# Performance work log

Hardware: AMD Instinct MI355X
Metric: run time of the kernel (lower is better)

## Reference

```python
import jax, jax.numpy as jnp
import numpy as np

EPS = 1e-4            # EDM2 normalize() epsilon
NUM_HEADS = 12
ATTN_BALANCE = 0.3
ROPE_BASE = 10000.0
NEG_INF = -1e9


def mp_weight(w):
    """EDM2 MPConv weight: per-output-channel normalize + magnitude-preserving scale.
    w: [out, in] (1x1 conv kernel squeezed)."""
    fan_in = w.shape[1]
    norm = jnp.linalg.norm(w, axis=1, keepdims=True)
    w = w / (EPS + norm * np.float32(np.sqrt(1.0 / fan_in)))  # normalize()
    return w * np.float32(1.0 / np.sqrt(fan_in))              # gain/sqrt(fan_in), gain=1


def apply_rope(q, k):
    """Rotary embedding over the frame index t. q,k: [b, m, t, hw, d]."""
    d = q.shape[-1]
    t = q.shape[2]
    inv_freq = 1.0 / (ROPE_BASE ** (jnp.arange(0, d, 2, dtype=jnp.float32) / d))
    ang = jnp.arange(t, dtype=jnp.float32)[:, None] * inv_freq[None, :]   # [t, d/2]
    cos = jnp.cos(ang)[None, None, :, None, :].astype(q.dtype)
    sin = jnp.sin(ang)[None, None, :, None, :].astype(q.dtype)

    def rot(x):
        x1, x2 = jnp.split(x, 2, axis=-1)
        return jnp.concatenate([x1 * cos - x2 * sin, x1 * sin + x2 * cos], axis=-1)

    return rot(q), rot(k)


def video_attention(x, w_qkv, w_proj, batch_size):
    bt, C, h, w_ = x.shape
    b = batch_size
    t = bt // b
    m = NUM_HEADS
    c = C // m
    hw = h * w_
    S = t * hw

    # MPConv QKV (1x1 conv == channel matmul)
    y = jnp.einsum('oi,bihw->bohw', mp_weight(w_qkv), x)   # [(b t), 3C, h, w]
    # '(b t) (s m c) h w -> s b m t (h w) c'
    y = y.reshape(b, t, 3, m, c, h, w_).transpose(2, 0, 3, 1, 5, 6, 4).reshape(3, b, m, t, hw, c)
    q, k, v = y[0], y[1], y[2]

    q, k = apply_rope(q, k)
    q = q.reshape(b, m, S, c)
    k = k.reshape(b, m, S, c)
    v = v.reshape(b, m, S, c)

    # block-causal video mask: token in frame i attends to all tokens of frames <= i
    frame = jnp.arange(S) // hw
    mask = frame[:, None] >= frame[None, :]                 # [S, S]

    scores = jnp.einsum('bmqc,bmkc->bmqk', q, k) * np.float32(1.0 / np.sqrt(c))
    scores = jnp.where(mask, scores, NEG_INF)
    attn = jax.nn.softmax(scores, axis=-1)
    yo = jnp.einsum('bmqk,bmkc->bmqc', attn, v)             # [b, m, S, c]

    # 'b m (t h w) c -> (b t) (c m) h w'
    yo = yo.reshape(b, m, t, h, w_, c).transpose(0, 2, 5, 1, 3, 4).reshape(bt, C, h, w_)
    yo = jnp.einsum('oi,bihw->bohw', mp_weight(w_proj), yo)

    # mp_sum(x, y, t=attn_balance)
    tb = ATTN_BALANCE
    scale = np.float32(1.0 / np.sqrt((1.0 - tb) ** 2 + tb ** 2))
    return (x * np.float32(1.0 - tb) + yo * np.float32(tb)) * scale


def setup_inputs() -> dict:
    key = jax.random.key(0)
    k1, k2, k3 = jax.random.split(key, 3)
    batch_size = 2
    n_frames = 8
    C, h, w = 768, 16, 16
    x = jax.random.normal(k1, (batch_size * n_frames, C, h, w), dtype=jnp.float32)
    w_qkv = jax.random.normal(k2, (3 * C, C), dtype=jnp.float32)
    w_proj = jax.random.normal(k3, (C, C), dtype=jnp.float32)
    return {"x": x, "w_qkv": w_qkv, "w_proj": w_proj, "batch_size": batch_size}


def reference(x, w_qkv, w_proj, batch_size):
    return video_attention(x, w_qkv, w_proj, batch_size)
```

## Files before the change

kernel.cpp:

```cpp
#include <hip/hip_runtime.h>

typedef __bf16 bf16_t;
typedef __bf16 bf16x4 __attribute__((ext_vector_type(4)));
typedef __bf16 bf16x8 __attribute__((ext_vector_type(8)));
typedef float  f32x4  __attribute__((ext_vector_type(4)));

static constexpr int NHEADS = 12, HC = 64, HW = 256, SEQ = 2048;
static constexpr size_t QKV_ONE = (size_t)2 * NHEADS * SEQ * HC;
static constexpr size_t NSTRIDE = 768 * 256;

__global__ __launch_bounds__(256) void va_prep(const float* __restrict__ wqkv,
                                               const float* __restrict__ wproj,
                                               const float* __restrict__ x,
                                               bf16_t* __restrict__ wout,
                                               bf16_t* __restrict__ xt) {
    int blk = blockIdx.x;
    if (blk < 3072) {
        int row = blk;
        bool is_proj = (row >= 2304);
        const float* wr = is_proj ? wproj + (size_t)(row - 2304) * 768
                                  : wqkv + (size_t)row * 768;
        float part = 0.f;
        for (int i = threadIdx.x; i < 768; i += 256) { float v = wr[i]; part += v * v; }
#pragma unroll
        for (int off = 32; off > 0; off >>= 1) part += __shfl_down(part, off, 64);
        __shared__ float red[4];
        if ((threadIdx.x & 63) == 0) red[threadIdx.x >> 6] = part;
        __syncthreads();
        if (threadIdx.x == 0) {
            float s = red[0] + red[1] + red[2] + red[3];
            red[0] = 1.0f / (2.7712813e-3f + sqrtf(s));
        }
        __syncthreads();
        float sc = red[0];
        for (int i = threadIdx.x; i < 768; i += 256) {
            int j = is_proj ? ((i % 12) * 64 + i / 12) : i;
            wout[(size_t)row * 768 + j] = (bf16_t)(wr[i] * sc);
        }
    } else {
        int t = blk - 3072;
        int n  = t & 15;
        int rest = t >> 4;
        int p0 = (rest & 7) * 32;
        int c0 = (rest >> 3) * 32;
        __shared__ float sm[32][33];
        int tx = threadIdx.x & 31, ty = threadIdx.x >> 5;
        const float* xp = x + (size_t)n * NSTRIDE;
#pragma unroll
        for (int i = 0; i < 4; i++)
            sm[ty + i * 8][tx] = xp[(size_t)(c0 + ty + i * 8) * 256 + p0 + tx];
        __syncthreads();
        bf16_t* xo = xt + (size_t)n * NSTRIDE;
#pragma unroll
        for (int i = 0; i < 4; i++)
            xo[(size_t)(p0 + ty + i * 8) * 768 + c0 + tx] = (bf16_t)sm[tx][ty + i * 8];
    }
}

__global__ __launch_bounds__(256, 2) void va_qkv_mfma(const bf16_t* __restrict__ Wb,
                                                      const bf16_t* __restrict__ xt,
                                                      bf16_t* __restrict__ qkvb) {
    int idx = blockIdx.x;
    int n  = (idx & 7) + 8 * ((idx >> 3) & 1);
    int rest = idx >> 4;
    int p0 = (rest & 1) * 128;
    int m0 = (rest >> 1) * 128;
    int tid = threadIdx.x;
    int lane = tid & 63, w = tid >> 6;
    int lo = lane & 15, hi = lane >> 4;
    int wm = w >> 1, wn = w & 1;
    int lx = lo & 7;

    __shared__ bf16_t Asm[128 * 64];
    __shared__ bf16_t Bsm[128 * 64];

    int srow = tid >> 3, schunk = tid & 7;
    const bf16_t* Ag = Wb + (size_t)(m0 + srow) * 768 + schunk * 8;
    const bf16_t* Bg = xt + (size_t)n * NSTRIDE + (size_t)(p0 + srow) * 768 + schunk * 8;
    int sdst = srow * 128 + ((schunk ^ (srow & 7)) << 4);

    f32x4 acc[4][4];
#pragma unroll
    for (int mt = 0; mt < 4; mt++)
#pragma unroll
        for (int nt = 0; nt < 4; nt++) acc[mt][nt] = (f32x4){0.f, 0.f, 0.f, 0.f};

    bf16x8 sa[4], sb[4];

    auto gload = [&](int k0) {
#pragma unroll
        for (int i = 0; i < 4; i++) {
            sa[i] = *(const bf16x8*)(Ag + (size_t)i * 32 * 768 + k0);
            sb[i] = *(const bf16x8*)(Bg + (size_t)i * 32 * 768 + k0);
        }
    };
    auto swrite = [&]() {
        char* Ac = (char*)Asm;
        char* Bc = (char*)Bsm;
#pragma unroll
        for (int i = 0; i < 4; i++) {
            *(bf16x8*)(Ac + sdst + i * 32 * 128) = sa[i];
            *(bf16x8*)(Bc + sdst + i * 32 * 128) = sb[i];
        }
    };

    gload(0);
    for (int s = 0; s < 12; s++) {
        __syncthreads();
        swrite();
        if (s < 11) gload((s + 1) * 64);
        __syncthreads();
#pragma unroll
        for (int kk = 0; kk < 64; kk += 32) {
            int cb = kk >> 3;
            bf16x8 af[4], bfr[4];
            const char* Ac = (const char*)Asm;
            const char* Bc = (const char*)Bsm;
#pragma unroll
            for (int mt = 0; mt < 4; mt++) {
                int row = wm * 64 + mt * 16 + lo;
                af[mt] = *(const bf16x8*)(Ac + row * 128 + (((cb + hi) ^ lx) << 4));
            }
#pragma unroll
            for (int nt = 0; nt < 4; nt++) {
                int row = wn * 64 + nt * 16 + lo;
                bfr[nt] = *(const bf16x8*)(Bc + row * 128 + (((cb + hi) ^ lx) << 4));
            }
#pragma unroll
            for (int mt = 0; mt < 4; mt++)
#pragma unroll
                for (int nt = 0; nt < 4; nt++)
                    acc[mt][nt] = __builtin_amdgcn_mfma_f32_16x16x32_bf16(af[mt], bfr[nt], acc[mt][nt], 0, 0, 0);
        }
    }

    int head_global = (m0 + wm * 64) >> 6;
    int qkv_idx = head_global / 12;
    int head    = head_global % 12;
    int b = n >> 3, tt = n & 7;
    int bm = b * 12 + head;
    if (qkv_idx < 2) {
        float qsc = (qkv_idx == 0) ? 0.18033688011f : 1.0f;
        float ttf = (float)tt;
#pragma unroll
        for (int mt = 0; mt < 2; mt++)
#pragma unroll
            for (int r = 0; r < 4; r++) {
                int j = mt * 16 + hi * 4 + r;
                float ang = ttf * __expf(-(float)j * 0.2878231366242557f);
                float cs = __cosf(ang), sn = __sinf(ang);
#pragma unroll
                for (int nt = 0; nt < 4; nt++) {
                    float x1 = acc[mt][nt][r], x2 = acc[mt + 2][nt][r];
                    acc[mt][nt][r]     = (x1 * cs - x2 * sn) * qsc;
                    acc[mt + 2][nt][r] = (x1 * sn + x2 * cs) * qsc;
                }
            }
        bf16_t* dst = qkvb + (size_t)qkv_idx * QKV_ONE + ((size_t)bm * SEQ + (size_t)tt * HW) * HC;
#pragma unroll
        for (int mt = 0; mt < 4; mt++)
#pragma unroll
            for (int nt = 0; nt < 4; nt++)
#pragma unroll
                for (int r = 0; r < 4; r++) {
                    int cc = mt * 16 + hi * 4 + r;
                    int p  = p0 + wn * 64 + nt * 16 + lo;
                    dst[(size_t)p * HC + cc] = (bf16_t)acc[mt][nt][r];
                }
    } else {
        bf16_t* dst = qkvb + 2 * QKV_ONE + (size_t)bm * HC * SEQ + (size_t)tt * HW;
#pragma unroll
        for (int mt = 0; mt < 4; mt++)
#pragma unroll
            for (int nt = 0; nt < 4; nt++)
#pragma unroll
                for (int r = 0; r < 4; r++) {
                    int cc = mt * 16 + hi * 4 + r;
                    int p  = p0 + wn * 64 + nt * 16 + lo;
                    dst[(size_t)cc * SEQ + p] = (bf16_t)acc[mt][nt][r];
                }
    }
}

__global__ __launch_bounds__(256, 2) void va_attn(const bf16_t* __restrict__ qkvb,
                                                  bf16_t* __restrict__ yob) {
    int s = blockIdx.x;
    int f = 7 - (s / 96);
    int within = s % 96;
    int bm = within % 24;
    int qs = within / 24;

    int tid = threadIdx.x;
    int w = tid >> 6, lane = tid & 63;
    int lo = lane & 15, hi = lane >> 4;
    int lx = lo & 7;

    const bf16_t* qbase = qkvb + (size_t)bm * SEQ * HC;
    const bf16_t* kbase = qkvb + QKV_ONE + (size_t)bm * SEQ * HC;
    const bf16_t* vbase = qkvb + 2 * QKV_ONE + (size_t)bm * HC * SEQ;

    __shared__ bf16_t PBF[4][64 * 64];
    __shared__ float  Lsm[4][64];
    bf16_t* PBw = PBF[w];

    const bf16_t* qrow = qbase + (size_t)(f * 256 + qs * 64 + lo) * HC;
    bf16x8 qf[4][2];
#pragma unroll
    for (int nq = 0; nq < 4; nq++) {
        qf[nq][0] = *(const bf16x8*)(qrow + (size_t)nq * 16 * HC + hi * 8);
        qf[nq][1] = *(const bf16x8*)(qrow + (size_t)nq * 16 * HC + 32 + hi * 8);
    }
    f32x4 o[4][4];
#pragma unroll
    for (int ct = 0; ct < 4; ct++)
#pragma unroll
        for (int nq = 0; nq < 4; nq++) o[ct][nq] = (f32x4){0.f, 0.f, 0.f, 0.f};
    float l4[4] = {0.f, 0.f, 0.f, 0.f};

    int kend = (f + 1) * 256;

    bf16x8 ka[8];
    {
        const bf16_t* kp = kbase + (size_t)(w * 64 + lo) * HC + hi * 8;
#pragma unroll
        for (int mt = 0; mt < 4; mt++) {
            ka[2 * mt]     = *(const bf16x8*)(kp + (size_t)mt * 16 * HC);
            ka[2 * mt + 1] = *(const bf16x8*)(kp + (size_t)mt * 16 * HC + 32);
        }
    }

    for (int kpos = w * 64; kpos < kend; kpos += 256) {
        const bf16_t* vp = vbase + (size_t)(lo) * SEQ + kpos + hi * 8;
        bf16x8 va[8];
#pragma unroll
        for (int ct = 0; ct < 4; ct++) {
            va[2 * ct]     = *(const bf16x8*)(vp + (size_t)ct * 16 * SEQ);
            va[2 * ct + 1] = *(const bf16x8*)(vp + (size_t)ct * 16 * SEQ + 32);
        }
        __builtin_amdgcn_s_setprio(1);
#pragma unroll
        for (int mt = 0; mt < 2; mt++) {
#pragma unroll
            for (int nq = 0; nq < 4; nq++) {
                f32x4 sacc = (f32x4){0.f, 0.f, 0.f, 0.f};
                sacc = __builtin_amdgcn_mfma_f32_16x16x32_bf16(ka[2 * mt], qf[nq][0], sacc, 0, 0, 0);
                sacc = __builtin_amdgcn_mfma_f32_16x16x32_bf16(ka[2 * mt + 1], qf[nq][1], sacc, 0, 0, 0);
                bf16x4 pk;
#pragma unroll
                for (int r = 0; r < 4; r++) {
                    float p;
                    asm("v_exp_f32 %0, %1" : "=v"(p) : "v"(sacc[r]));
                    l4[nq] += p;
                    pk[r] = (bf16_t)p;
                }
                *(bf16x4*)(PBw + (nq * 16 + lo) * 64 +
                           (((2 * mt + (hi >> 1)) ^ lx) * 8) + (hi & 1) * 4) = pk;
            }
        }
        __builtin_amdgcn_s_setprio(0);
        bf16x8 pb0[4], pb1[4];
#pragma unroll
        for (int nq = 0; nq < 4; nq++)
            pb0[nq] = *(const bf16x8*)(PBw + (nq * 16 + lo) * 64 + (hi ^ lx) * 8);
        __builtin_amdgcn_s_setprio(1);
#pragma unroll
        for (int mt = 2; mt < 4; mt++) {
#pragma unroll
            for (int nq = 0; nq < 4; nq++) {
                f32x4 sacc = (f32x4){0.f, 0.f, 0.f, 0.f};
                sacc = __builtin_amdgcn_mfma_f32_16x16x32_bf16(ka[2 * mt], qf[nq][0], sacc, 0, 0, 0);
                sacc = __builtin_amdgcn_mfma_f32_16x16x32_bf16(ka[2 * mt + 1], qf[nq][1], sacc, 0, 0, 0);
                bf16x4 pk;
#pragma unroll
                for (int r = 0; r < 4; r++) {
                    float p;
                    asm("v_exp_f32 %0, %1" : "=v"(p) : "v"(sacc[r]));
                    l4[nq] += p;
                    pk[r] = (bf16_t)p;
                }
                *(bf16x4*)(PBw + (nq * 16 + lo) * 64 +
                           (((2 * mt + (hi >> 1)) ^ lx) * 8) + (hi & 1) * 4) = pk;
            }
        }
        __builtin_amdgcn_s_setprio(0);
        int knext = (kpos + 256 < kend) ? kpos + 256 : kpos;
        bf16x8 kan[8];
        {
            const bf16_t* kp = kbase + (size_t)(knext + lo) * HC + hi * 8;
#pragma unroll
            for (int mt = 0; mt < 4; mt++) {
                kan[2 * mt]     = *(const bf16x8*)(kp + (size_t)mt * 16 * HC);
                kan[2 * mt + 1] = *(const bf16x8*)(kp + (size_t)mt * 16 * HC + 32);
            }
        }
#pragma unroll
        for (int nq = 0; nq < 4; nq++)
            pb1[nq] = *(const bf16x8*)(PBw + (nq * 16 + lo) * 64 + ((4 + hi) ^ lx) * 8);
        __builtin_amdgcn_s_setprio(1);
#pragma unroll
        for (int ct = 0; ct < 4; ct++)
#pragma unroll
            for (int nq = 0; nq < 4; nq++)
                o[ct][nq] = __builtin_amdgcn_mfma_f32_16x16x32_bf16(va[2 * ct], pb0[nq], o[ct][nq], 0, 0, 0);
#pragma unroll
        for (int ct = 0; ct < 4; ct++)
#pragma unroll
            for (int nq = 0; nq < 4; nq++)
                o[ct][nq] = __builtin_amdgcn_mfma_f32_16x16x32_bf16(va[2 * ct + 1], pb1[nq], o[ct][nq], 0, 0, 0);
        __builtin_amdgcn_s_setprio(0);
#pragma unroll
        for (int i = 0; i < 8; i++) ka[i] = kan[i];
    }
#pragma unroll
    for (int nq = 0; nq < 4; nq++) {
        l4[nq] += __shfl_xor(l4[nq], 16, 64);
        l4[nq] += __shfl_xor(l4[nq], 32, 64);
    }
    if (hi == 0) {
#pragma unroll
        for (int nq = 0; nq < 4; nq++) Lsm[w][nq * 16 + lo] = l4[nq];
    }
#pragma unroll
    for (int ct = 0; ct < 4; ct++)
#pragma unroll
        for (int nq = 0; nq < 4; nq++) {
            bf16x4 ov;
#pragma unroll
            for (int r = 0; r < 4; r++) ov[r] = (bf16_t)o[ct][nq][r];
            *(bf16x4*)(PBw + (nq * 16 + lo) * 64 +
                       (((2 * ct + (hi >> 1)) ^ lx) * 8) + (hi & 1) * 4) = ov;
        }
    __syncthreads();
    int head = bm % 12, b = bm / 12;
    bf16_t* yb = yob + (size_t)(b * 8 + f) * NSTRIDE + (size_t)(qs * 64) * 768 + head * 64;
#pragma unroll
    for (int i = 0; i < 2; i++) {
        int c = i * 256 + tid;
        int row = c >> 3, j = c & 7;
        int off = row * 64 + ((j ^ (row & 7)) * 8);
        float invl = 1.0f / (Lsm[0][row] + Lsm[1][row] + Lsm[2][row] + Lsm[3][row]);
        bf16x8 p0 = *(const bf16x8*)(PBF[0] + off);
        bf16x8 p1 = *(const bf16x8*)(PBF[1] + off);
        bf16x8 p2 = *(const bf16x8*)(PBF[2] + off);
        bf16x8 p3 = *(const bf16x8*)(PBF[3] + off);
        bf16x8 o8;
#pragma unroll
        for (int r = 0; r < 8; r++)
            o8[r] = (bf16_t)(((float)p0[r] + (float)p1[r] + (float)p2[r] + (float)p3[r]) * invl);
        *(bf16x8*)(yb + (size_t)row * 768 + j * 8) = o8;
    }
}

__global__ __launch_bounds__(256, 2) void va_proj_mfma(const bf16_t* __restrict__ Wb,
                                                       const bf16_t* __restrict__ yob,
                                                       const float* __restrict__ x,
                                                       float* __restrict__ out) {
    int idx = blockIdx.x;
    int n  = (idx & 7) + 8 * ((idx >> 3) & 1);
    int rest = idx >> 4;
    int p0 = (rest & 1) * 128;
    int m0 = (rest >> 1) * 64;
    int tid = threadIdx.x;
    int lane = tid & 63, w = tid >> 6;
    int lo = lane & 15, hi = lane >> 4;
    int lx = lo & 7;

    __shared__ bf16_t Asm[64 * 64];
    __shared__ bf16_t Bsm[128 * 64];

    int srow = tid >> 3, schunk = tid & 7;
    const bf16_t* Ag = Wb + (size_t)(m0 + srow) * 768 + schunk * 8;
    const bf16_t* Bg = yob + (size_t)n * NSTRIDE + (size_t)(p0 + srow) * 768 + schunk * 8;
    int sdst = srow * 128 + ((schunk ^ (srow & 7)) << 4);

    f32x4 acc[4][2];
#pragma unroll
    for (int mt = 0; mt < 4; mt++)
#pragma unroll
        for (int nt = 0; nt < 2; nt++) acc[mt][nt] = (f32x4){0.f, 0.f, 0.f, 0.f};

    bf16x8 sa[2], sb[4];
    auto gload = [&](int k0) {
#pragma unroll
        for (int i = 0; i < 2; i++)
            sa[i] = *(const bf16x8*)(Ag + (size_t)i * 32 * 768 + k0);
#pragma unroll
        for (int i = 0; i < 4; i++)
            sb[i] = *(const bf16x8*)(Bg + (size_t)i * 32 * 768 + k0);
    };
    auto swrite = [&]() {
        char* Ac = (char*)Asm;
        char* Bc = (char*)Bsm;
#pragma unroll
        for (int i = 0; i < 2; i++)
            *(bf16x8*)(Ac + sdst + i * 32 * 128) = sa[i];
#pragma unroll
        for (int i = 0; i < 4; i++)
            *(bf16x8*)(Bc + sdst + i * 32 * 128) = sb[i];
    };

    gload(0);
    for (int s = 0; s < 12; s++) {
        __syncthreads();
        swrite();
        if (s < 11) gload((s + 1) * 64);
        __syncthreads();
#pragma unroll
        for (int kk = 0; kk < 64; kk += 32) {
            int cb = kk >> 3;
            bf16x8 af[4], bfr[2];
            const char* Ac = (const char*)Asm;
            const char* Bc = (const char*)Bsm;
#pragma unroll
            for (int mt = 0; mt < 4; mt++) {
                int row = mt * 16 + lo;
                af[mt] = *(const bf16x8*)(Ac + row * 128 + (((cb + hi) ^ lx) << 4));
            }
#pragma unroll
            for (int nt = 0; nt < 2; nt++) {
                int row = w * 32 + nt * 16 + lo;
                bfr[nt] = *(const bf16x8*)(Bc + row * 128 + (((cb + hi) ^ lx) << 4));
            }
#pragma unroll
            for (int mt = 0; mt < 4; mt++)
#pragma unroll
                for (int nt = 0; nt < 2; nt++)
                    acc[mt][nt] = __builtin_amdgcn_mfma_f32_16x16x32_bf16(af[mt], bfr[nt], acc[mt][nt], 0, 0, 0);
        }
    }

    const float* xn = x + (size_t)n * NSTRIDE;
    float* on = out + (size_t)n * NSTRIDE;
#pragma unroll
    for (int mt = 0; mt < 4; mt++)
#pragma unroll
        for (int nt = 0; nt < 2; nt++)
#pragma unroll
            for (int r = 0; r < 4; r++) {
                int oo = m0 + mt * 16 + hi * 4 + r;
                int p  = p0 + w * 32 + nt * 16 + lo;
                size_t idx2 = (size_t)oo * 256 + p;
                on[idx2] = (xn[idx2] * 0.7f + acc[mt][nt][r] * 0.3f) * 1.3130643f;
            }
}

extern "C" void kernel_launch(void* const* d_in, const int* in_sizes, int n_in,
                              void* d_out, int out_size, void* d_ws, size_t ws_size,
                              hipStream_t stream) {
    const float* x     = (const float*)d_in[0];
    const float* wqkv  = (const float*)d_in[1];
    const float* wproj = (const float*)d_in[2];
    float* out = (float*)d_out;

    bf16_t* Opart = (bf16_t*)d_ws;
    float*  lpart = (float*)(Opart + (size_t)24 * 36 * 16384);
    bf16_t* wqkv_nb  = (bf16_t*)(lpart + (size_t)24 * 36 * 256);
    bf16_t* xt       = wqkv_nb + (size_t)3072 * 768;
    bf16_t* qkvb     = xt + NSTRIDE * 16;
    bf16_t* yob      = qkvb + 3 * QKV_ONE;

    va_prep<<<6144, 256, 0, stream>>>(wqkv, wproj, x, wqkv_nb, xt);
    va_qkv_mfma<<<576, 256, 0, stream>>>(wqkv_nb, xt, qkvb);
    va_attn<<<768, 256, 0, stream>>>(qkvb, yob);
    va_proj_mfma<<<384, 256, 0, stream>>>(wqkv_nb + (size_t)2304 * 768, yob, x, out);
}
```

Measured before the change: 151.2 us.

## Use direct global-to-LDS loads with double buffering in QKV and proj GEMMs

```diff
diff --git a/kernel.cpp b/kernel.cpp
--- a/kernel.cpp
+++ b/kernel.cpp
@@ -8,6 +8,12 @@
 static constexpr int NHEADS = 12, HC = 64, HW = 256, SEQ = 2048;
 static constexpr size_t QKV_ONE = (size_t)2 * NHEADS * SEQ * HC;
 static constexpr size_t NSTRIDE = 768 * 256;
+
+__device__ __forceinline__ void gload_lds16(const bf16_t* g, bf16_t* l) {
+    __builtin_amdgcn_global_load_lds(
+        (const __attribute__((address_space(1))) void*)g,
+        (__attribute__((address_space(3))) void*)l, 16, 0, 0);
+}
 
 __global__ __launch_bounds__(256) void va_prep(const float* __restrict__ wqkv,
                                                const float* __restrict__ wproj,
@@ -71,13 +77,22 @@
     int wm = w >> 1, wn = w & 1;
     int lx = lo & 7;
 
-    __shared__ bf16_t Asm[128 * 64];
-    __shared__ bf16_t Bsm[128 * 64];
-
-    int srow = tid >> 3, schunk = tid & 7;
-    const bf16_t* Ag = Wb + (size_t)(m0 + srow) * 768 + schunk * 8;
-    const bf16_t* Bg = xt + (size_t)n * NSTRIDE + (size_t)(p0 + srow) * 768 + schunk * 8;
-    int sdst = srow * 128 + ((schunk ^ (srow & 7)) << 4);
+    __shared__ bf16_t Asm[2][128 * 64];
+    __shared__ bf16_t Bsm[2][128 * 64];
+
+    int r8 = lane >> 3;
+    int csw = (lane & 7) ^ r8;
+    const bf16_t* Ags = Wb + (size_t)(m0 + w * 32 + r8) * 768 + csw * 8;
+    const bf16_t* Bgs = xt + (size_t)n * NSTRIDE + (size_t)(p0 + w * 32 + r8) * 768 + csw * 8;
+
+    auto stage = [&](int s, int buf) {
+        int k0 = s * 64;
+#pragma unroll
+        for (int i = 0; i < 4; i++) {
+            gload_lds16(Ags + (size_t)i * 8 * 768 + k0, &Asm[buf][(w * 32 + i * 8) * 64]);
+            gload_lds16(Bgs + (size_t)i * 8 * 768 + k0, &Bsm[buf][(w * 32 + i * 8) * 64]);
+        }
+    };
 
     f32x4 acc[4][4];
 #pragma unroll
@@ -85,37 +100,17 @@
 #pragma unroll
         for (int nt = 0; nt < 4; nt++) acc[mt][nt] = (f32x4){0.f, 0.f, 0.f, 0.f};
 
-    bf16x8 sa[4], sb[4];
-
-    auto gload = [&](int k0) {
-#pragma unroll
-        for (int i = 0; i < 4; i++) {
-            sa[i] = *(const bf16x8*)(Ag + (size_t)i * 32 * 768 + k0);
-            sb[i] = *(const bf16x8*)(Bg + (size_t)i * 32 * 768 + k0);
-        }
-    };
-    auto swrite = [&]() {
-        char* Ac = (char*)Asm;
-        char* Bc = (char*)Bsm;
-#pragma unroll
-        for (int i = 0; i < 4; i++) {
-            *(bf16x8*)(Ac + sdst + i * 32 * 128) = sa[i];
-            *(bf16x8*)(Bc + sdst + i * 32 * 128) = sb[i];
-        }
-    };
-
-    gload(0);
+    stage(0, 0);
+    __syncthreads();
     for (int s = 0; s < 12; s++) {
-        __syncthreads();
-        swrite();
-        if (s < 11) gload((s + 1) * 64);
-        __syncthreads();
+        int buf = s & 1;
+        if (s < 11) stage(s + 1, buf ^ 1);
 #pragma unroll
         for (int kk = 0; kk < 64; kk += 32) {
             int cb = kk >> 3;
             bf16x8 af[4], bfr[4];
-            const char* Ac = (const char*)Asm;
-            const char* Bc = (const char*)Bsm;
+            const char* Ac = (const char*)Asm[buf];
+            const char* Bc = (const char*)Bsm[buf];
 #pragma unroll
             for (int mt = 0; mt < 4; mt++) {
                 int row = wm * 64 + mt * 16 + lo;
@@ -132,6 +127,7 @@
                 for (int nt = 0; nt < 4; nt++)
                     acc[mt][nt] = __builtin_amdgcn_mfma_f32_16x16x32_bf16(af[mt], bfr[nt], acc[mt][nt], 0, 0, 0);
         }
+        __syncthreads();
     }
 
     int head_global = (m0 + wm * 64) >> 6;
@@ -365,13 +361,23 @@
     int lo = lane & 15, hi = lane >> 4;
     int lx = lo & 7;
 
-    __shared__ bf16_t Asm[64 * 64];
-    __shared__ bf16_t Bsm[128 * 64];
-
-    int srow = tid >> 3, schunk = tid & 7;
-    const bf16_t* Ag = Wb + (size_t)(m0 + srow) * 768 + schunk * 8;
-    const bf16_t* Bg = yob + (size_t)n * NSTRIDE + (size_t)(p0 + srow) * 768 + schunk * 8;
-    int sdst = srow * 128 + ((schunk ^ (srow & 7)) << 4);
+    __shared__ bf16_t Asm[2][64 * 64];
+    __shared__ bf16_t Bsm[2][128 * 64];
+
+    int r8 = lane >> 3;
+    int csw = (lane & 7) ^ r8;
+    const bf16_t* Ags = Wb + (size_t)(m0 + w * 16 + r8) * 768 + csw * 8;
+    const bf16_t* Bgs = yob + (size_t)n * NSTRIDE + (size_t)(p0 + w * 32 + r8) * 768 + csw * 8;
+
+    auto stage = [&](int s, int buf) {
+        int k0 = s * 64;
+#pragma unroll
+        for (int i = 0; i < 2; i++)
+            gload_lds16(Ags + (size_t)i * 8 * 768 + k0, &Asm[buf][(w * 16 + i * 8) * 64]);
+#pragma unroll
+        for (int i = 0; i < 4; i++)
+            gload_lds16(Bgs + (size_t)i * 8 * 768 + k0, &Bsm[buf][(w * 32 + i * 8) * 64]);
+    };
 
     f32x4 acc[4][2];
 #pragma unroll
@@ -379,38 +385,17 @@
 #pragma unroll
         for (int nt = 0; nt < 2; nt++) acc[mt][nt] = (f32x4){0.f, 0.f, 0.f, 0.f};
 
-    bf16x8 sa[2], sb[4];
-    auto gload = [&](int k0) {
-#pragma unroll
-        for (int i = 0; i < 2; i++)
-            sa[i] = *(const bf16x8*)(Ag + (size_t)i * 32 * 768 + k0);
-#pragma unroll
-        for (int i = 0; i < 4; i++)
-            sb[i] = *(const bf16x8*)(Bg + (size_t)i * 32 * 768 + k0);
-    };
-    auto swrite = [&]() {
-        char* Ac = (char*)Asm;
-        char* Bc = (char*)Bsm;
-#pragma unroll
-        for (int i = 0; i < 2; i++)
-            *(bf16x8*)(Ac + sdst + i * 32 * 128) = sa[i];
-#pragma unroll
-        for (int i = 0; i < 4; i++)
-            *(bf16x8*)(Bc + sdst + i * 32 * 128) = sb[i];
-    };
-
-    gload(0);
+    stage(0, 0);
+    __syncthreads();
     for (int s = 0; s < 12; s++) {
-        __syncthreads();
-        swrite();
-        if (s < 11) gload((s + 1) * 64);
-        __syncthreads();
+        int buf = s & 1;
+        if (s < 11) stage(s + 1, buf ^ 1);
 #pragma unroll
         for (int kk = 0; kk < 64; kk += 32) {
             int cb = kk >> 3;
             bf16x8 af[4], bfr[2];
-            const char* Ac = (const char*)Asm;
-            const char* Bc = (const char*)Bsm;
+            const char* Ac = (const char*)Asm[buf];
+            const char* Bc = (const char*)Bsm[buf];
 #pragma unroll
             for (int mt = 0; mt < 4; mt++) {
                 int row = mt * 16 + lo;
@@ -427,6 +412,7 @@
                 for (int nt = 0; nt < 2; nt++)
                     acc[mt][nt] = __builtin_amdgcn_mfma_f32_16x16x32_bf16(af[mt], bfr[nt], acc[mt][nt], 0, 0, 0);
         }
+        __syncthreads();
     }
 
     const float* xn = x + (size_t)n * NSTRIDE;
```

After: 163.9 us. 8.4% more time.
